# Performance work log

Hardware: AMD Instinct MI355X
Metric: run time of the kernel (lower is better)

The kernel has to match this reference:

```python
import jax, jax.numpy as jnp
import numpy as np

VOCAB = 1400
EPS = 1e-06


def _cross_entropy(logits, targets, num_classes, ignore_index=-100):
    # logits: [N, C], targets: [N] int
    logits = logits.reshape(-1, num_classes)
    targets = targets.reshape(-1)
    logp = jax.nn.log_softmax(logits, axis=-1)
    valid = targets != ignore_index
    safe_t = jnp.where(valid, targets, 0)
    nll = -jnp.take_along_axis(logp, safe_t[:, None], axis=-1)[:, 0]
    nll = jnp.where(valid, nll, 0.0)
    denom = jnp.maximum(valid.sum(), 1)
    return nll.sum() / denom


def _concordance_loss(pred_survival, true_times, events):
    # pred_survival: [n, T]; true_times: [n]; events: [n] in {0,1}
    n = pred_survival.shape[0]
    m = pred_survival.mean(axis=1)  # [n]
    i_lt_j = jnp.triu(jnp.ones((n, n), dtype=bool), k=1)  # pairs with i < j
    valid = i_lt_j & (events[:, None] == 1) & (true_times[:, None] < true_times[None, :])
    score = jnp.where(m[:, None] < m[None, :], 1.0,
                      jnp.where(m[:, None] == m[None, :], 0.5, 0.0))
    num_pairs = valid.sum()
    conc = jnp.where(valid, score, 0.0).sum()
    return jnp.where(num_pairs > 0, 1.0 - conc / jnp.maximum(num_pairs, 1), 0.0)


def setup_inputs() -> dict:
    key = jax.random.key(0)
    ks = jax.random.split(key, 10)
    B, S = 8, 2048
    n, T = 4096, 120
    return {
        "disease_logits": jax.random.normal(ks[0], (B, S, VOCAB), jnp.float32),
        "disease_targets": jax.random.randint(ks[1], (B, S), 0, VOCAB, jnp.int64),
        "time_to_event": jax.random.uniform(ks[2], (B, S), jnp.float32),
        "time_targets": jax.random.uniform(ks[3], (B, S), jnp.float32),
        "risk_stratification": jax.random.normal(ks[4], (B, S, 5), jnp.float32),
        "risk_targets": jax.random.randint(ks[5], (B, S), 0, 5, jnp.int64),
        "survival_curves": jax.random.uniform(ks[6], (n, T), jnp.float32),
        "survival_targets": jax.random.uniform(ks[7], (n,), jnp.float32),
        "event_indicators": jax.random.randint(ks[8], (n,), 0, 2, jnp.int32),
        "uncertainty": jax.random.uniform(ks[9], (B, S), jnp.float32),
    }


def reference(disease_logits, disease_targets, time_to_event, time_targets,
              risk_stratification, risk_targets, survival_curves,
              survival_targets, event_indicators, uncertainty):
    disease = _cross_entropy(disease_logits, disease_targets, VOCAB, ignore_index=-100)
    rates = 1.0 / (time_to_event + EPS)
    time_loss = -jnp.mean(jnp.log(rates + EPS) - rates * time_targets)
    risk = _cross_entropy(risk_stratification, risk_targets, 5, ignore_index=-100)
    survival = _concordance_loss(survival_curves, survival_targets, event_indicators)
    unc = jnp.mean(uncertainty) * 0.01
    total = disease + time_loss + risk + survival + unc
    # [disease, time, risk, survival, uncertainty, total]
    return jnp.stack([disease, time_loss, risk, survival, unc, total])
```

## Files before the change

### kernel.cpp

```cpp
#include <hip/hip_runtime.h>
#include <math.h>

#define VOCAB   1400
#define NROWS   16384
#define NSURV   4096
#define TSURV   120
#define LEPS    1e-6f

#define NF4     350

#define NB_CE    2048
#define NB_M     1024
#define NB_SMALL 64
#define NB_CONC  512

#define WS_M        0
#define WS_DNLL     4096
#define WS_DCNT     6144
#define WS_CONC     8192
#define WS_PAIRS    8704
#define WS_TIME     9216
#define WS_RNLL     9280
#define WS_RCNT     9344
#define WS_UNC      9408

__device__ __forceinline__ float wave_sum(float v) {
#pragma unroll
    for (int off = 32; off >= 1; off >>= 1) v += __shfl_xor(v, off);
    return v;
}

__global__ __launch_bounds__(256) void kA_fused(
    const float* __restrict__ logits, const int* __restrict__ tgt,
    const float* __restrict__ tte,    const float* __restrict__ ttgt,
    const float* __restrict__ risk,   const int* __restrict__ rtgt,
    const float* __restrict__ surv,   const float* __restrict__ unc,
    float* __restrict__ ws)
{
    const int b    = blockIdx.x;
    const int tid  = threadIdx.x;
    const int lane = tid & 63;
    const int wid  = tid >> 6;
    __shared__ float sred[16];

    if (b < NB_CE) {
        const int row0 = b * 8 + wid * 2;
        const float4* rp0 = reinterpret_cast<const float4*>(logits + (size_t)row0 * VOCAB);
        const float4* rp1 = reinterpret_cast<const float4*>(logits + (size_t)(row0 + 1) * VOCAB);
        const int t0 = tgt[row0];
        const int t1 = tgt[row0 + 1];

        float4 a[6], c[6];
#pragma unroll
        for (int k = 0; k < 6; ++k) {
            const int idx = lane + k * 64;
            a[k] = (idx < NF4) ? rp0[idx]
                               : make_float4(-INFINITY, -INFINITY, -INFINITY, -INFINITY);
        }
#pragma unroll
        for (int k = 0; k < 6; ++k) {
            const int idx = lane + k * 64;
            c[k] = (idx < NF4) ? rp1[idx]
                               : make_float4(-INFINITY, -INFINITY, -INFINITY, -INFINITY);
        }

        float s0 = 0.f, x0 = 0.f;
#pragma unroll
        for (int k = 0; k < 6; ++k) {
            const int base = (lane + k * 64) * 4;
            const float e0 = a[k].x, e1 = a[k].y, e2 = a[k].z, e3 = a[k].w;
            s0 += expf(e0) + expf(e1) + expf(e2) + expf(e3);
            x0 += (base + 0 == t0) ? e0 : 0.f;
            x0 += (base + 1 == t0) ? e1 : 0.f;
            x0 += (base + 2 == t0) ? e2 : 0.f;
            x0 += (base + 3 == t0) ? e3 : 0.f;
        }
        s0 = wave_sum(s0);
        x0 = wave_sum(x0);

        float s1 = 0.f, x1 = 0.f;
#pragma unroll
        for (int k = 0; k < 6; ++k) {
            const int base = (lane + k * 64) * 4;
            const float e0 = c[k].x, e1 = c[k].y, e2 = c[k].z, e3 = c[k].w;
            s1 += expf(e0) + expf(e1) + expf(e2) + expf(e3);
            x1 += (base + 0 == t1) ? e0 : 0.f;
            x1 += (base + 1 == t1) ? e1 : 0.f;
            x1 += (base + 2 == t1) ? e2 : 0.f;
            x1 += (base + 3 == t1) ? e3 : 0.f;
        }
        s1 = wave_sum(s1);
        x1 = wave_sum(x1);

        if (lane == 0) {
            float nll = 0.f, valid = 0.f;
            if (t0 != -100) { nll += logf(s0) - x0; valid += 1.f; }
            if (t1 != -100) { nll += logf(s1) - x1; valid += 1.f; }
            sred[wid]     = nll;
            sred[4 + wid] = valid;
        }
        __syncthreads();
        if (tid == 0) {
            ws[WS_DNLL + b] = sred[0] + sred[1] + sred[2] + sred[3];
            ws[WS_DCNT + b] = sred[4] + sred[5] + sred[6] + sred[7];
        }
    } else if (b < NB_CE + NB_M) {
        const int row = (b - NB_CE) * 4 + wid;
        const float* rp = surv + (size_t)row * TSURV;
        float s = rp[lane];
        if (lane < TSURV - 64) s += rp[lane + 64];
        s = wave_sum(s);
        if (lane == 0) ws[WS_M + row] = s * (1.0f / TSURV);
    } else {
        const int bb = b - NB_CE - NB_M;
        const int i  = bb * 256 + tid;

        const float t    = tte[i];
        const float rate = 1.0f / (t + LEPS);
        const float tterm = logf(rate + LEPS) - rate * ttgt[i];
        const float u = unc[i];
        const float* rr = risk + (size_t)i * 5;
        const float r0 = rr[0], r1 = rr[1], r2 = rr[2], r3 = rr[3], r4 = rr[4];
        const float rm = fmaxf(fmaxf(fmaxf(r0, r1), fmaxf(r2, r3)), r4);
        const float rs = expf(r0 - rm) + expf(r1 - rm) + expf(r2 - rm)
                       + expf(r3 - rm) + expf(r4 - rm);
        float rnll = 0.f, rcnt = 0.f;
        const int rt = rtgt[i];
        if (rt != -100) {
            rnll = (rm + logf(rs)) - rr[rt];
            rcnt = 1.f;
        }

        float a0 = wave_sum(tterm);
        float a1 = wave_sum(rnll);
        float a2 = wave_sum(rcnt);
        float a3 = wave_sum(u);
        if (lane == 0) {
            sred[wid * 4 + 0] = a0; sred[wid * 4 + 1] = a1;
            sred[wid * 4 + 2] = a2; sred[wid * 4 + 3] = a3;
        }
        __syncthreads();
        if (tid == 0) {
            ws[WS_TIME + bb] = sred[0] + sred[4] + sred[8]  + sred[12];
            ws[WS_RNLL + bb] = sred[1] + sred[5] + sred[9]  + sred[13];
            ws[WS_RCNT + bb] = sred[2] + sred[6] + sred[10] + sred[14];
            ws[WS_UNC  + bb] = sred[3] + sred[7] + sred[11] + sred[15];
        }
    }
}

__global__ __launch_bounds__(256) void k2_concordance(
    const float* __restrict__ stgt, const int* __restrict__ ev,
    float* __restrict__ ws)
{
    const int bid  = blockIdx.x;
    const int tid  = threadIdx.x;
    const int lane = tid & 63;
    const int wid  = tid >> 6;
    __shared__ float sred[8];

    float conc = 0.f, pairs = 0.f;
#pragma unroll
    for (int s = 0; s < 8; ++s) {
        const int i = bid + s * NB_CONC;
        if (ev[i] != 1) continue;
        const float ti = stgt[i];
        const float mi = ws[WS_M + i];
        for (int j = i + 1 + tid; j < NSURV; j += 256) {
            const float tj = stgt[j];
            if (ti < tj) {
                pairs += 1.f;
                const float mj = ws[WS_M + j];
                conc += (mi < mj) ? 1.f : ((mi == mj) ? 0.5f : 0.f);
            }
        }
    }
    conc  = wave_sum(conc);
    pairs = wave_sum(pairs);
    if (lane == 0) { sred[wid] = conc; sred[4 + wid] = pairs; }
    __syncthreads();
    if (tid == 0) {
        ws[WS_CONC  + bid] = sred[0] + sred[1] + sred[2] + sred[3];
        ws[WS_PAIRS + bid] = sred[4] + sred[5] + sred[6] + sred[7];
    }
}

__global__ __launch_bounds__(256) void k3_finalize(
    const float* __restrict__ ws, float* __restrict__ out)
{
    const int tid  = threadIdx.x;
    const int lane = tid & 63;
    const int wid  = tid >> 6;
    __shared__ float sm[4][8];

    float dn = 0.f, dc = 0.f;
    for (int k = tid; k < NB_CE; k += 256) {
        dn += ws[WS_DNLL + k];
        dc += ws[WS_DCNT + k];
    }
    float cc = 0.f, pp = 0.f;
    for (int k = tid; k < NB_CONC; k += 256) {
        cc += ws[WS_CONC  + k];
        pp += ws[WS_PAIRS + k];
    }
    float ts = 0.f, rn = 0.f, rc = 0.f, us = 0.f;
    if (tid < 64) {
        ts = ws[WS_TIME + tid];
        rn = ws[WS_RNLL + tid];
        rc = ws[WS_RCNT + tid];
        us = ws[WS_UNC  + tid];
    }
    dn = wave_sum(dn); dc = wave_sum(dc); cc = wave_sum(cc); pp = wave_sum(pp);
    ts = wave_sum(ts); rn = wave_sum(rn); rc = wave_sum(rc); us = wave_sum(us);
    if (lane == 0) {
        sm[wid][0] = dn; sm[wid][1] = dc; sm[wid][2] = cc; sm[wid][3] = pp;
        sm[wid][4] = ts; sm[wid][5] = rn; sm[wid][6] = rc; sm[wid][7] = us;
    }
    __syncthreads();
    if (tid == 0) {
        dn = sm[0][0] + sm[1][0] + sm[2][0] + sm[3][0];
        dc = sm[0][1] + sm[1][1] + sm[2][1] + sm[3][1];
        cc = sm[0][2] + sm[1][2] + sm[2][2] + sm[3][2];
        pp = sm[0][3] + sm[1][3] + sm[2][3] + sm[3][3];
        ts = sm[0][4] + sm[1][4] + sm[2][4] + sm[3][4];
        rn = sm[0][5] + sm[1][5] + sm[2][5] + sm[3][5];
        rc = sm[0][6] + sm[1][6] + sm[2][6] + sm[3][6];
        us = sm[0][7] + sm[1][7] + sm[2][7] + sm[3][7];

        const float disease   = dn / fmaxf(dc, 1.f);
        const float time_loss = -(ts * (1.0f / 16384.f));
        const float risk_loss = rn / fmaxf(rc, 1.f);
        const float survival  = (pp > 0.f) ? (1.f - cc / fmaxf(pp, 1.f)) : 0.f;
        const float uncer     = us * (1.0f / 16384.f) * 0.01f;

        out[0] = disease;
        out[1] = time_loss;
        out[2] = risk_loss;
        out[3] = survival;
        out[4] = uncer;
        out[5] = disease + time_loss + risk_loss + survival + uncer;
    }
}

extern "C" void kernel_launch(void* const* d_in, const int* in_sizes, int n_in,
                              void* d_out, int out_size, void* d_ws, size_t ws_size,
                              hipStream_t stream)
{
    const float* logits = (const float*)d_in[0];
    const int*   tgt    = (const int*)  d_in[1];
    const float* tte    = (const float*)d_in[2];
    const float* ttgt   = (const float*)d_in[3];
    const float* risk   = (const float*)d_in[4];
    const int*   rtgt   = (const int*)  d_in[5];
    const float* surv   = (const float*)d_in[6];
    const float* stgt   = (const float*)d_in[7];
    const int*   ev     = (const int*)  d_in[8];
    const float* unc    = (const float*)d_in[9];
    float*       out    = (float*)d_out;
    float*       ws     = (float*)d_ws;

    kA_fused<<<NB_CE + NB_M + NB_SMALL, 256, 0, stream>>>(
        logits, tgt, tte, ttgt, risk, rtgt, surv, unc, ws);
    k2_concordance<<<NB_CONC, 256, 0, stream>>>(stgt, ev, ws);
    k3_finalize<<<1, 256, 0, stream>>>(ws, out);
}
```

Baseline: 173.2 us.

## Use one row per wave for CE, direct target gather, and LDS-staged concordance inputs

The cross-entropy branch now handles one row per wave instead of two, doubling the CE block count and resizing the workspace offsets to match. The target logit is read with a single direct load rather than compared against every element during the sweep. The concordance kernel stages all survival targets and mean values into shared memory before the pair loop, replacing repeated global reads. This lowers register pressure and ALU work in the CE path but adds 32KB of LDS per concordance block plus a full staging pass in each of 512 blocks.

```diff
diff --git a/kernel.cpp b/kernel.cpp
--- a/kernel.cpp
+++ b/kernel.cpp
@@ -9,20 +9,20 @@
 
 #define NF4     350
 
-#define NB_CE    2048
+#define NB_CE    4096
 #define NB_M     1024
 #define NB_SMALL 64
 #define NB_CONC  512
 
 #define WS_M        0
 #define WS_DNLL     4096
-#define WS_DCNT     6144
-#define WS_CONC     8192
-#define WS_PAIRS    8704
-#define WS_TIME     9216
-#define WS_RNLL     9280
-#define WS_RCNT     9344
-#define WS_UNC      9408
+#define WS_DCNT     8192
+#define WS_CONC     12288
+#define WS_PAIRS    12800
+#define WS_TIME     13312
+#define WS_RNLL     13376
+#define WS_RCNT     13440
+#define WS_UNC      13504
 
 __device__ __forceinline__ float wave_sum(float v) {
 #pragma unroll
@@ -44,58 +44,29 @@
     __shared__ float sred[16];
 
     if (b < NB_CE) {
-        const int row0 = b * 8 + wid * 2;
-        const float4* rp0 = reinterpret_cast<const float4*>(logits + (size_t)row0 * VOCAB);
-        const float4* rp1 = reinterpret_cast<const float4*>(logits + (size_t)(row0 + 1) * VOCAB);
-        const int t0 = tgt[row0];
-        const int t1 = tgt[row0 + 1];
-
-        float4 a[6], c[6];
+        const int row = b * 4 + wid;
+        const float4* rp = reinterpret_cast<const float4*>(logits + (size_t)row * VOCAB);
+        const int t = tgt[row];
+        const float xtv = (t != -100) ? logits[(size_t)row * VOCAB + t] : 0.f;
+
+        float4 a[6];
 #pragma unroll
         for (int k = 0; k < 6; ++k) {
             const int idx = lane + k * 64;
-            a[k] = (idx < NF4) ? rp0[idx]
+            a[k] = (idx < NF4) ? rp[idx]
                                : make_float4(-INFINITY, -INFINITY, -INFINITY, -INFINITY);
         }
+
+        float s = 0.f;
 #pragma unroll
         for (int k = 0; k < 6; ++k) {
-            const int idx = lane + k * 64;
-            c[k] = (idx < NF4) ? rp1[idx]
-                               : make_float4(-INFINITY, -INFINITY, -INFINITY, -INFINITY);
-        }
-
-        float s0 = 0.f, x0 = 0.f;
-#pragma unroll
-        for (int k = 0; k < 6; ++k) {
-            const int base = (lane + k * 64) * 4;
-            const float e0 = a[k].x, e1 = a[k].y, e2 = a[k].z, e3 = a[k].w;
-            s0 += expf(e0) + expf(e1) + expf(e2) + expf(e3);
-            x0 += (base + 0 == t0) ? e0 : 0.f;
-            x0 += (base + 1 == t0) ? e1 : 0.f;
-            x0 += (base + 2 == t0) ? e2 : 0.f;
-            x0 += (base + 3 == t0) ? e3 : 0.f;
-        }
-        s0 = wave_sum(s0);
-        x0 = wave_sum(x0);
-
-        float s1 = 0.f, x1 = 0.f;
-#pragma unroll
-        for (int k = 0; k < 6; ++k) {
-            const int base = (lane + k * 64) * 4;
-            const float e0 = c[k].x, e1 = c[k].y, e2 = c[k].z, e3 = c[k].w;
-            s1 += expf(e0) + expf(e1) + expf(e2) + expf(e3);
-            x1 += (base + 0 == t1) ? e0 : 0.f;
-            x1 += (base + 1 == t1) ? e1 : 0.f;
-            x1 += (base + 2 == t1) ? e2 : 0.f;
-            x1 += (base + 3 == t1) ? e3 : 0.f;
-        }
-        s1 = wave_sum(s1);
-        x1 = wave_sum(x1);
+            s += expf(a[k].x) + expf(a[k].y) + expf(a[k].z) + expf(a[k].w);
+        }
+        s = wave_sum(s);
 
         if (lane == 0) {
             float nll = 0.f, valid = 0.f;
-            if (t0 != -100) { nll += logf(s0) - x0; valid += 1.f; }
-            if (t1 != -100) { nll += logf(s1) - x1; valid += 1.f; }
+            if (t != -100) { nll = logf(s) - xtv; valid = 1.f; }
             sred[wid]     = nll;
             sred[4 + wid] = valid;
         }
@@ -157,20 +128,28 @@
     const int tid  = threadIdx.x;
     const int lane = tid & 63;
     const int wid  = tid >> 6;
+    __shared__ float sh_t[NSURV];
+    __shared__ float sh_m[NSURV];
     __shared__ float sred[8];
+
+    for (int k = tid; k < NSURV; k += 256) {
+        sh_t[k] = stgt[k];
+        sh_m[k] = ws[WS_M + k];
+    }
+    __syncthreads();
 
     float conc = 0.f, pairs = 0.f;
 #pragma unroll
     for (int s = 0; s < 8; ++s) {
         const int i = bid + s * NB_CONC;
         if (ev[i] != 1) continue;
-        const float ti = stgt[i];
-        const float mi = ws[WS_M + i];
+        const float ti = sh_t[i];
+        const float mi = sh_m[i];
         for (int j = i + 1 + tid; j < NSURV; j += 256) {
-            const float tj = stgt[j];
+            const float tj = sh_t[j];
             if (ti < tj) {
                 pairs += 1.f;
-                const float mj = ws[WS_M + j];
+                const float mj = sh_m[j];
                 conc += (mi < mj) ? 1.f : ((mi == mj) ? 0.5f : 0.f);
             }
         }
```

Result: faster. 169.4 us (-2.2%).
